# Optimization experiments

Hardware: AMD Instinct MI355X
Metric: run time of the kernel (lower is better)

## Reference

```python
import jax, jax.numpy as jnp
import numpy as np
import math

N_HEAD_FULL = 16  # config.n_head

def setup_inputs() -> dict:
    key = jax.random.key(0)
    ks = jax.random.split(key, 5)
    B, T, D = 2, 4096, 1024
    scale = 1.0 / math.sqrt(D)
    x = jax.random.normal(ks[0], (B, T, D), dtype=jnp.float32)
    wq = jax.random.normal(ks[1], (D, D), dtype=jnp.float32) * scale
    wk = jax.random.normal(ks[2], (D, D), dtype=jnp.float32) * scale
    wv = jax.random.normal(ks[3], (D, D), dtype=jnp.float32) * scale
    wo = jax.random.normal(ks[4], (D, D), dtype=jnp.float32) * scale
    return {"x": x, "wq": wq, "wk": wk, "wv": wv, "wo": wo, "active_dim": 512}

def reference(x, wq, wk, wv, wo, active_dim):
    B, T, D = x.shape
    ad = int(active_dim)
    n_head = max(1, ad * N_HEAD_FULL // D)
    head_dim = ad // n_head
    xs = x[:, :, :ad]
    # F.linear(x, W[:ad,:ad]) == x @ W[:ad,:ad].T
    q = xs @ wq[:ad, :ad].T
    k = xs @ wk[:ad, :ad].T
    v = xs @ wv[:ad, :ad].T
    q = q.reshape(B, T, n_head, head_dim).transpose(0, 2, 1, 3)  # [B,H,T,hd]
    k = k.reshape(B, T, n_head, head_dim).transpose(0, 2, 1, 3)
    v = v.reshape(B, T, n_head, head_dim).transpose(0, 2, 1, 3)
    attn = jnp.einsum('bhqd,bhkd->bhqk', q, k) / math.sqrt(head_dim)
    # kv_cache=None -> T_k=T, triu diagonal = T_k-T+1 = 1 -> strict causal mask
    mask = jnp.triu(jnp.ones((T, T), dtype=bool), k=1)
    attn = jnp.where(mask, -jnp.inf, attn)
    attn = jax.nn.softmax(attn, axis=-1)
    out = jnp.einsum('bhqk,bhkd->bhqd', attn, v)
    out = out.transpose(0, 2, 1, 3).reshape(B, T, ad)
    out = out @ wo[:ad, :ad].T
    return jnp.pad(out, ((0, 0), (0, 0), (0, D - ad)))
```

## Files before the change

kernel.cpp:

```cpp
#include <hip/hip_runtime.h>
#include <hip/hip_bf16.h>
#include <stdint.h>


typedef __bf16 bf16;
typedef bf16  bf16x8 __attribute__((ext_vector_type(8)));
typedef bf16  bf16x4v __attribute__((ext_vector_type(4)));
typedef float f32x4  __attribute__((ext_vector_type(4)));
typedef uint32_t u32x4 __attribute__((ext_vector_type(4)));

#define SCL 0.18033688011112042f
#define NEG_BIG (-30000.0f)

static __device__ __forceinline__ f32x4 mfma_bf16(bf16x8 a, bf16x8 b, f32x4 c) {
    return __builtin_amdgcn_mfma_f32_16x16x32_bf16(a, b, c, 0, 0, 0);
}

static __device__ __forceinline__ void gl_lds(const bf16* g, bf16* l) {
    __builtin_amdgcn_global_load_lds(
        (const __attribute__((address_space(1))) uint32_t*)(g),
        (__attribute__((address_space(3))) uint32_t*)(l), 16, 0, 0);
}

__global__ __launch_bounds__(256) void sniff_dtype(
    const uint16_t* __restrict__ x, int* __restrict__ flag)
{
    __shared__ int cnt;
    if (threadIdx.x == 0) cnt = 0;
    __syncthreads();
    int local = 0;
    for (int i = threadIdx.x; i < 2048; i += 256) {
        const int e = (x[i] >> 7) & 0xFF;
        if (e >= 0xC0) ++local;
    }
    if (local) atomicAdd(&cnt, local);
    __syncthreads();
    if (threadIdx.x == 0) *flag = (cnt >= 8) ? 1 : 0;
}

__global__ __launch_bounds__(256) void convert_all(
    const void* __restrict__ x,
    const void* __restrict__ wq, const void* __restrict__ wk,
    const void* __restrict__ wv, const void* __restrict__ wo,
    bf16* __restrict__ xb, bf16* __restrict__ wb,
    const int* __restrict__ flag)
{
    const int bid = blockIdx.x;
    const void* src;
    bf16* dst;
    int sub;
    if (bid < 2048) { src = x; dst = xb; sub = bid; }
    else {
        const int w = bid - 2048;
        const int wsel = w >> 7;
        src = (wsel == 0) ? wq : (wsel == 1) ? wk : (wsel == 2) ? wv : wo;
        dst = wb + (size_t)wsel * 262144;
        sub = w & 127;
    }
    const int i = (sub * 256 + threadIdx.x) * 8;
    const int r = i >> 9, c = i & 511;
    bf16x8 v;
    if (*flag) {
        const float* s = (const float*)src + (size_t)r * 1024 + c;
        f32x4 f0 = *(const f32x4*)s;
        f32x4 f1 = *(const f32x4*)(s + 4);
#pragma unroll
        for (int j = 0; j < 4; ++j) { v[j] = (bf16)f0[j]; v[4 + j] = (bf16)f1[j]; }
    } else {
        v = *(const bf16x8*)((const bf16*)src + (size_t)r * 1024 + c);
    }
    *(bf16x8*)(dst + (size_t)r * 512 + c) = v;
}

__global__ __launch_bounds__(256) void gemm_qkv(
    const bf16* __restrict__ A, const bf16* __restrict__ B,
    bf16* __restrict__ Qb, bf16* __restrict__ Kb, bf16* __restrict__ Vb)
{
    const int bx   = blockIdx.x;
    const int n0   = bx * 128;
    const int m0   = blockIdx.y * 128;
    const int wave = threadIdx.x >> 6;
    const int lane = threadIdx.x & 63;
    const int col  = lane & 15;
    const int quad = lane >> 4;
    const int wr   = wave >> 1, wc = wave & 1;

    __shared__ __align__(16) bf16 As[2][128][64];
    __shared__ __align__(16) bf16 Bs[2][128][64];

    const int rr = lane >> 3, cc = lane & 7;
    const int cs = (cc ^ rr) * 8;

    auto stage = [&](int kt, int buf) {
#pragma unroll
        for (int j = 0; j < 4; ++j) {
            const int r0 = wave * 32 + j * 8;
            gl_lds(A + (size_t)(m0 + r0 + rr) * 512 + kt * 64 + cs, &As[buf][r0][0]);
            gl_lds(B + (size_t)(n0 + r0 + rr) * 512 + kt * 64 + cs, &Bs[buf][r0][0]);
        }
    };

    f32x4 acc[4][4];
#pragma unroll
    for (int m = 0; m < 4; ++m)
#pragma unroll
        for (int n = 0; n < 4; ++n)
#pragma unroll
            for (int r = 0; r < 4; ++r) acc[m][n][r] = 0.0f;

    stage(0, 0);
    asm volatile("s_waitcnt vmcnt(0)" ::: "memory");
    __syncthreads();

    for (int kt = 0; kt < 8; ++kt) {
        const int buf = kt & 1;
        if (kt + 1 < 8) stage(kt + 1, buf ^ 1);

#pragma unroll
        for (int kk = 0; kk < 2; ++kk) {
            bf16x8 af[4], bfr[4];
#pragma unroll
            for (int m = 0; m < 4; ++m) {
                const int row = wr * 64 + m * 16 + col;
                af[m] = *(const bf16x8*)&As[buf][row][(((kk << 2) + quad) ^ (col & 7)) * 8];
            }
#pragma unroll
            for (int n = 0; n < 4; ++n) {
                const int row = wc * 64 + n * 16 + col;
                bfr[n] = *(const bf16x8*)&Bs[buf][row][(((kk << 2) + quad) ^ (col & 7)) * 8];
            }
#pragma unroll
            for (int m = 0; m < 4; ++m)
#pragma unroll
                for (int n = 0; n < 4; ++n)
                    acc[m][n] = mfma_bf16(af[m], bfr[n], acc[m][n]);
        }

        asm volatile("s_waitcnt vmcnt(0)" ::: "memory");
        __syncthreads();
    }

    const int bb = m0 >> 12;

    if (bx < 8) {
        bf16* __restrict__ dst = (bx < 4) ? Qb : Kb;
        const float qs = (bx < 4) ? SCL : 1.0f;
#pragma unroll
        for (int m = 0; m < 4; ++m) {
#pragma unroll
            for (int n = 0; n < 4; ++n) {
#pragma unroll
                for (int r = 0; r < 4; ++r) {
                    const int row = m0 + wr * 64 + m * 16 + quad * 4 + r;
                    const int cnl = (n0 & 511) + wc * 64 + n * 16 + col;
                    const int t = row & 4095;
                    const int h = cnl >> 6, d = cnl & 63;
                    dst[((size_t)(bb * 8 + h) * 4096 + t) * 64 + d] = (bf16)(acc[m][n][r] * qs);
                }
            }
        }
    } else {
        const int h0 = (n0 - 1024) >> 6;
#pragma unroll
        for (int m = 0; m < 4; ++m) {
#pragma unroll
            for (int n = 0; n < 4; ++n) {
                bf16x4v pk;
#pragma unroll
                for (int r = 0; r < 4; ++r) pk[r] = (bf16)acc[m][n][r];
                const int d  = wc * 64 + n * 16 + col;
                const int t  = (m0 & 4095) + wr * 64 + m * 16 + quad * 4;
                *(bf16x4v*)(Vb + ((size_t)(bb * 8 + h0 + (d >> 6)) * 64 + (d & 63)) * 4096 + t) = pk;
            }
        }
    }
}

__global__ __launch_bounds__(256) void gemm_out_pad(
    const bf16* __restrict__ A, const bf16* __restrict__ B, void* __restrict__ C,
    const int* __restrict__ flag)
{
    const int bx  = blockIdx.x;
    const int m0  = blockIdx.y * 128;
    const int isf = *flag;

    if (bx >= 4) {
        const int c0  = 512 + (bx - 4) * 128;
        const int row = m0 + (threadIdx.x >> 1);
        const int cb  = (threadIdx.x & 1) * 64;
        if (isf) {
            float* p = (float*)C + (size_t)row * 1024 + c0 + cb;
            f32x4 z; z[0] = 0.f; z[1] = 0.f; z[2] = 0.f; z[3] = 0.f;
#pragma unroll
            for (int j = 0; j < 16; ++j) *(f32x4*)(p + j * 4) = z;
        } else {
            bf16* p = (bf16*)C + (size_t)row * 1024 + c0 + cb;
            u32x4 z; z[0] = 0u; z[1] = 0u; z[2] = 0u; z[3] = 0u;
#pragma unroll
            for (int j = 0; j < 8; ++j) *(u32x4*)(p + j * 8) = z;
        }
        return;
    }

    const int n0   = bx * 128;
    const int wave = threadIdx.x >> 6;
    const int lane = threadIdx.x & 63;
    const int col  = lane & 15;
    const int quad = lane >> 4;
    const int wr   = wave >> 1, wc = wave & 1;

    __shared__ __align__(16) bf16 As[2][128][64];
    __shared__ __align__(16) bf16 Bs[2][128][64];

    const int rr = lane >> 3, cc = lane & 7;
    const int cs = (cc ^ rr) * 8;

    auto stage = [&](int kt, int buf) {
#pragma unroll
        for (int j = 0; j < 4; ++j) {
            const int r0 = wave * 32 + j * 8;
            gl_lds(A + (size_t)(m0 + r0 + rr) * 512 + kt * 64 + cs, &As[buf][r0][0]);
            gl_lds(B + (size_t)(n0 + r0 + rr) * 512 + kt * 64 + cs, &Bs[buf][r0][0]);
        }
    };

    f32x4 acc[4][4];
#pragma unroll
    for (int m = 0; m < 4; ++m)
#pragma unroll
        for (int n = 0; n < 4; ++n)
#pragma unroll
            for (int r = 0; r < 4; ++r) acc[m][n][r] = 0.0f;

    stage(0, 0);
    asm volatile("s_waitcnt vmcnt(0)" ::: "memory");
    __syncthreads();

    for (int kt = 0; kt < 8; ++kt) {
        const int buf = kt & 1;
        if (kt + 1 < 8) stage(kt + 1, buf ^ 1);

#pragma unroll
        for (int kk = 0; kk < 2; ++kk) {
            bf16x8 af[4], bfr[4];
#pragma unroll
            for (int m = 0; m < 4; ++m) {
                const int row = wr * 64 + m * 16 + col;
                af[m] = *(const bf16x8*)&As[buf][row][(((kk << 2) + quad) ^ (col & 7)) * 8];
            }
#pragma unroll
            for (int n = 0; n < 4; ++n) {
                const int row = wc * 64 + n * 16 + col;
                bfr[n] = *(const bf16x8*)&Bs[buf][row][(((kk << 2) + quad) ^ (col & 7)) * 8];
            }
#pragma unroll
            for (int m = 0; m < 4; ++m)
#pragma unroll
                for (int n = 0; n < 4; ++n)
                    acc[m][n] = mfma_bf16(af[m], bfr[n], acc[m][n]);
        }

        asm volatile("s_waitcnt vmcnt(0)" ::: "memory");
        __syncthreads();
    }

#pragma unroll
    for (int m = 0; m < 4; ++m) {
#pragma unroll
        for (int n = 0; n < 4; ++n) {
#pragma unroll
            for (int r = 0; r < 4; ++r) {
                const int row = m0 + wr * 64 + m * 16 + quad * 4 + r;
                const int cn  = n0 + wc * 64 + n * 16 + col;
                const float f = acc[m][n][r];
                if (isf) ((float*)C)[(size_t)row * 1024 + cn] = f;
                else     ((bf16*)C)[(size_t)row * 1024 + cn] = (bf16)f;
            }
        }
    }
}

template<int NSPLIT>
__global__ __launch_bounds__(256) void flash_kernel(
    const bf16* __restrict__ Q, const bf16* __restrict__ K,
    const bf16* __restrict__ Vt,
    float* __restrict__ Opart, float* __restrict__ Spart)
{
    const int wave = threadIdx.x >> 6;
    const int lane = threadIdx.x & 63;
    const int qc   = lane & 15;
    const int quad = lane >> 4;

    const int bh  = blockIdx.x & 15;
    const int qb0 = (blockIdx.x >> 4) & 15;
    const int s   = blockIdx.x >> 8;

    const int STEPS = 66 / NSPLIT;
    const int g0 = STEPS * s, g1 = g0 + STEPS;

    const bf16* __restrict__ Qh = Q  + (size_t)bh * (4096 * 64);
    const bf16* __restrict__ Kh = K  + (size_t)bh * (4096 * 64);
    const bf16* __restrict__ Vh = Vt + (size_t)bh * (64 * 4096);

    __shared__ __align__(16) bf16 Ksh[2][64][64];
    __shared__ __align__(16) bf16 Vsh[2][64][64];
    __shared__ __align__(16) bf16 Plds[4][2][16][72];

    const int h   = qc & 7;
    const int swz = (quad ^ h) * 8;
    const bf16* kB  = &Ksh[0][qc][swz];
    const bf16* kB2 = &Ksh[0][qc][swz ^ 32];
    const bf16* vB  = &Vsh[0][qc][swz];
    const bf16* vB2 = &Vsh[0][qc][swz ^ 32];
    bf16*       pwA = &Plds[wave][0][qc][quad * 4];
    const bf16* prA = &Plds[wave][0][qc][quad * 8];

    const int rr = lane >> 3, cc = lane & 7;
    const int cs = (cc ^ rr) * 8;

    bf16x8 vones;
#pragma unroll
    for (int j = 0; j < 8; ++j) vones[j] = (bf16)1.0f;

    auto stage = [&](int kb, int buf) {
#pragma unroll
        for (int j = 0; j < 2; ++j) {
            const int r0 = wave * 16 + j * 8;
            gl_lds(Kh + (size_t)(kb * 64 + r0 + rr) * 64 + cs, &Ksh[buf][r0][0]);
            gl_lds(Vh + (size_t)(r0 + rr) * 4096 + kb * 64 + cs, &Vsh[buf][r0][0]);
        }
    };

    for (int chunk = 0; chunk < 2; ++chunk) {
        const int qb  = chunk ? (31 - qb0) : qb0;
        const int n0t = 2 * qb0 + 2;
        const int n1t = 64 - 2 * qb0;
        int k0, k1;
        if (chunk == 0) {
            k0 = (g0 > 0) ? g0 : 0;
            k1 = (g1 < n0t) ? g1 : n0t;
        } else {
            const int a = g0 - n0t, b2 = g1 - n0t;
            k0 = (a > 0) ? a : 0;
            k1 = (b2 < n1t) ? b2 : n1t;
        }

        const int qrow   = qb * 128 + wave * 32;
        const int ktmaxw = 2 * qb + (wave >> 1);

        bf16x8 aqA0 = *(const bf16x8*)(Qh + (size_t)(qrow + qc) * 64 + quad * 8);
        bf16x8 aqA1 = *(const bf16x8*)(Qh + (size_t)(qrow + qc) * 64 + 32 + quad * 8);
        bf16x8 aqB0 = *(const bf16x8*)(Qh + (size_t)(qrow + 16 + qc) * 64 + quad * 8);
        bf16x8 aqB1 = *(const bf16x8*)(Qh + (size_t)(qrow + 16 + qc) * 64 + 32 + quad * 8);

        f32x4 oA[4], oB[4], saccA, saccB;
#pragma unroll
        for (int r = 0; r < 4; ++r) { saccA[r] = 0.f; saccB[r] = 0.f; }
#pragma unroll
        for (int nt = 0; nt < 4; ++nt)
#pragma unroll
            for (int r = 0; r < 4; ++r) { oA[nt][r] = 0.f; oB[nt][r] = 0.f; }

        auto body = [&](const int kb, const int buf) {
            if (kb <= ktmaxw) {
                const bool diag = (kb == ktmaxw);

#pragma unroll
                for (int nt = 0; nt < 4; ++nt) {
                    bf16x8 kf0 = *(const bf16x8*)(kB  + buf * 4096 + nt * 1024);
                    bf16x8 kf1 = *(const bf16x8*)(kB2 + buf * 4096 + nt * 1024);

                    f32x4 sA; sA[0] = 0.f; sA[1] = 0.f; sA[2] = 0.f; sA[3] = 0.f;
                    sA = mfma_bf16(kf0, aqA0, sA);
                    sA = mfma_bf16(kf1, aqA1, sA);
                    f32x4 sB; sB[0] = 0.f; sB[1] = 0.f; sB[2] = 0.f; sB[3] = 0.f;
                    sB = mfma_bf16(kf0, aqB0, sB);
                    sB = mfma_bf16(kf1, aqB1, sB);

                    bf16x4v pkA, pkB;
#pragma unroll
                    for (int r2 = 0; r2 < 4; ++r2) {
                        float vA = sA[r2];
                        float vBv = sB[r2];
                        if (diag) {
                            const int kg = kb * 64 + nt * 16 + quad * 4 + r2;
                            if (kg > qrow + qc)      vA  = NEG_BIG;
                            if (kg > qrow + 16 + qc) vBv = NEG_BIG;
                        }
                        pkA[r2] = (bf16)__builtin_amdgcn_exp2f(vA);
                        pkB[r2] = (bf16)__builtin_amdgcn_exp2f(vBv);
                    }
                    *(bf16x4v*)(pwA + nt * 16)        = pkA;
                    *(bf16x4v*)(pwA + 1152 + nt * 16) = pkB;
                }

#pragma unroll
                for (int ks = 0; ks < 2; ++ks) {
                    bf16x8 apA = *(const bf16x8*)(prA + ks * 32);
                    bf16x8 apB = *(const bf16x8*)(prA + 1152 + ks * 32);
#pragma unroll
                    for (int nt = 0; nt < 4; ++nt) {
                        bf16x8 vf = *(const bf16x8*)((ks ? vB2 : vB) + buf * 4096 + nt * 1024);
                        oA[nt] = mfma_bf16(apA, vf, oA[nt]);
                        oB[nt] = mfma_bf16(apB, vf, oB[nt]);
                    }
                    saccA = mfma_bf16(apA, vones, saccA);
                    saccB = mfma_bf16(apB, vones, saccB);
                }
            }
        };

        if (k0 < k1) {
            stage(k0, 0);
            asm volatile("s_waitcnt vmcnt(0)" ::: "memory");
            __syncthreads();

            int kb = k0;
            while (true) {
                if (kb + 1 < k1) stage(kb + 1, 1);
                body(kb, 0);
                asm volatile("s_waitcnt vmcnt(0)" ::: "memory");
                __syncthreads();
                ++kb; if (kb >= k1) break;

                if (kb + 1 < k1) stage(kb + 1, 0);
                body(kb, 1);
                asm volatile("s_waitcnt vmcnt(0)" ::: "memory");
                __syncthreads();
                ++kb; if (kb >= k1) break;
            }
        }

        const int pw = (qb * 16 + bh) * NSPLIT + s;
        float* op = Opart + (size_t)pw * 8192 + (size_t)(wave * 32) * 64;
#pragma unroll
        for (int nt = 0; nt < 4; ++nt)
#pragma unroll
            for (int r = 0; r < 4; ++r) {
                op[(quad * 4 + r) * 64 + nt * 16 + qc]        = oA[nt][r];
                op[1024 + (quad * 4 + r) * 64 + nt * 16 + qc] = oB[nt][r];
            }
        if (qc == 0) {
            float* sp = Spart + (size_t)pw * 128 + wave * 32;
#pragma unroll
            for (int r = 0; r < 4; ++r) {
                sp[quad * 4 + r]      = saccA[r];
                sp[16 + quad * 4 + r] = saccB[r];
            }
        }
    }
}

template<int NSPLIT>
__global__ __launch_bounds__(256) void combine_kernel(
    const float* __restrict__ Opart, const float* __restrict__ Spart,
    bf16* __restrict__ Ob)
{
    const int u  = blockIdx.x;
    const int qb = u >> 4;
    const int bh = u & 15;
    const int c  = threadIdx.x & 63;
    const int g  = threadIdx.x >> 6;
    const int b = bh >> 3, h = bh & 7;

    const float* o0 = Opart + (size_t)(u * NSPLIT) * 8192;
    const float* s0 = Spart + (size_t)(u * NSPLIT) * 128;

#pragma unroll 4
    for (int rr = 0; rr < 32; ++rr) {
        const int row = g * 32 + rr;
        float ssum = 0.f, osum = 0.f;
#pragma unroll
        for (int j = 0; j < NSPLIT; ++j) {
            ssum += s0[j * 128 + row];
            osum += o0[(size_t)j * 8192 + row * 64 + c];
        }
        const float v = osum / ssum;
        const int t = qb * 128 + row;
        Ob[((size_t)b * 4096 + t) * 512 + h * 64 + c] = (bf16)v;
    }
}

extern "C" void kernel_launch(void* const* d_in, const int* in_sizes, int n_in,
                              void* d_out, int out_size, void* d_ws, size_t ws_size,
                              hipStream_t stream)
{
    (void)in_sizes; (void)n_in; (void)out_size;
    const void* x  = d_in[0];
    const void* wq = d_in[1];
    const void* wk = d_in[2];
    const void* wv = d_in[3];
    const void* wo = d_in[4];

    char* wsb = (char*)d_ws;
    bf16* xb   = (bf16*)(wsb + 0);
    bf16* Ob   = (bf16*)(wsb + 0);
    bf16* wb   = (bf16*)(wsb + 8388608);
    bf16* wob  = wb + 3 * 262144;
    bf16* Qb   = (bf16*)(wsb + 10485760);
    bf16* Kb   = (bf16*)(wsb + 18874368);
    bf16* Vb   = (bf16*)(wsb + 27262976);
    int*  flag = (int*) (wsb + 35651584);

    const size_t need3 = 35651600ull + (size_t)512 * 3 * (8192 + 128) * 4;
    const int nsplit = (ws_size >= need3) ? 3 : 2;

    float* Opart = (float*)(wsb + 35651600);
    float* Spart = (float*)(wsb + 35651600 + (size_t)512 * nsplit * 8192 * 4);

    const dim3 blk(256);

    sniff_dtype<<<1, blk, 0, stream>>>((const uint16_t*)x, flag);
    convert_all<<<2560, blk, 0, stream>>>(x, wq, wk, wv, wo, xb, wb, flag);

    gemm_qkv<<<dim3(12, 64), blk, 0, stream>>>(xb, wb, Qb, Kb, Vb);

    if (nsplit == 3) {
        flash_kernel<3><<<dim3(768), blk, 0, stream>>>(Qb, Kb, Vb, Opart, Spart);
        combine_kernel<3><<<dim3(512), blk, 0, stream>>>(Opart, Spart, Ob);
    } else {
        flash_kernel<2><<<dim3(512), blk, 0, stream>>>(Qb, Kb, Vb, Opart, Spart);
        combine_kernel<2><<<dim3(512), blk, 0, stream>>>(Opart, Spart, Ob);
    }

    gemm_out_pad<<<dim3(8, 64), blk, 0, stream>>>(Ob, wob, d_out, flag);
}
```

Baseline: 205.4 us.

## Fuse dtype sniff into convert and split-K combine into flash kernel

The dtype detection is now done redundantly by every convert block, which removes the separate sniff kernel launch, and block 1 also zeroes a set of per-tile counters. The split-KV combine step moves into the flash kernel's epilogue: each split bumps an atomic counter, and the last one to finish for a tile does the normalisation and writes Ob. This drops two kernel launches and their gaps in exchange for extra syncthreads and atomics in the flash epilogue, plus an extra 2048 bytes of workspace, which can change the nsplit choice.

Measured after the change: 264.0 us. +28.5%, slower.

```diff
diff --git a/kernel.cpp b/kernel.cpp
--- a/kernel.cpp
+++ b/kernel.cpp
@@ -22,30 +22,32 @@
         (__attribute__((address_space(3))) uint32_t*)(l), 16, 0, 0);
 }
 
-__global__ __launch_bounds__(256) void sniff_dtype(
-    const uint16_t* __restrict__ x, int* __restrict__ flag)
-{
-    __shared__ int cnt;
-    if (threadIdx.x == 0) cnt = 0;
-    __syncthreads();
-    int local = 0;
-    for (int i = threadIdx.x; i < 2048; i += 256) {
-        const int e = (x[i] >> 7) & 0xFF;
-        if (e >= 0xC0) ++local;
-    }
-    if (local) atomicAdd(&cnt, local);
-    __syncthreads();
-    if (threadIdx.x == 0) *flag = (cnt >= 8) ? 1 : 0;
-}
-
 __global__ __launch_bounds__(256) void convert_all(
     const void* __restrict__ x,
     const void* __restrict__ wq, const void* __restrict__ wk,
     const void* __restrict__ wv, const void* __restrict__ wo,
     bf16* __restrict__ xb, bf16* __restrict__ wb,
-    const int* __restrict__ flag)
+    int* __restrict__ flag, int* __restrict__ cnt)
 {
+    __shared__ int scnt;
+    if (threadIdx.x == 0) scnt = 0;
+    __syncthreads();
+    {
+        const uint16_t* xu = (const uint16_t*)x;
+        int local = 0;
+        for (int i = threadIdx.x; i < 2048; i += 256) {
+            const int e = (xu[i] >> 7) & 0xFF;
+            if (e >= 0xC0) ++local;
+        }
+        if (local) atomicAdd(&scnt, local);
+    }
+    __syncthreads();
+    const int isf = (scnt >= 8) ? 1 : 0;
+
     const int bid = blockIdx.x;
+    if (bid == 0 && threadIdx.x == 0) *flag = isf;
+    if (bid == 1) { cnt[threadIdx.x] = 0; cnt[threadIdx.x + 256] = 0; }
+
     const void* src;
     bf16* dst;
     int sub;
@@ -60,7 +62,7 @@
     const int i = (sub * 256 + threadIdx.x) * 8;
     const int r = i >> 9, c = i & 511;
     bf16x8 v;
-    if (*flag) {
+    if (isf) {
         const float* s = (const float*)src + (size_t)r * 1024 + c;
         f32x4 f0 = *(const f32x4*)s;
         f32x4 f1 = *(const f32x4*)(s + 4);
@@ -284,7 +286,8 @@
 __global__ __launch_bounds__(256) void flash_kernel(
     const bf16* __restrict__ Q, const bf16* __restrict__ K,
     const bf16* __restrict__ Vt,
-    float* __restrict__ Opart, float* __restrict__ Spart)
+    float* __restrict__ Opart, float* __restrict__ Spart,
+    bf16* __restrict__ Ob, int* __restrict__ cnt)
 {
     const int wave = threadIdx.x >> 6;
     const int lane = threadIdx.x & 63;
@@ -305,6 +308,7 @@
     __shared__ __align__(16) bf16 Ksh[2][64][64];
     __shared__ __align__(16) bf16 Vsh[2][64][64];
     __shared__ __align__(16) bf16 Plds[4][2][16][72];
+    __shared__ int tick;
 
     const int h   = qc & 7;
     const int swz = (quad ^ h) * 8;
@@ -431,7 +435,8 @@
             }
         }
 
-        const int pw = (qb * 16 + bh) * NSPLIT + s;
+        const int u  = qb * 16 + bh;
+        const int pw = u * NSPLIT + s;
         float* op = Opart + (size_t)pw * 8192 + (size_t)(wave * 32) * 64;
 #pragma unroll
         for (int nt = 0; nt < 4; ++nt)
@@ -448,36 +453,33 @@
                 sp[16 + quad * 4 + r] = saccB[r];
             }
         }
-    }
-}
-
-template<int NSPLIT>
-__global__ __launch_bounds__(256) void combine_kernel(
-    const float* __restrict__ Opart, const float* __restrict__ Spart,
-    bf16* __restrict__ Ob)
-{
-    const int u  = blockIdx.x;
-    const int qb = u >> 4;
-    const int bh = u & 15;
-    const int c  = threadIdx.x & 63;
-    const int g  = threadIdx.x >> 6;
-    const int b = bh >> 3, h = bh & 7;
-
-    const float* o0 = Opart + (size_t)(u * NSPLIT) * 8192;
-    const float* s0 = Spart + (size_t)(u * NSPLIT) * 128;
-
+
+        __syncthreads();
+        if (threadIdx.x == 0)
+            tick = __hip_atomic_fetch_add(&cnt[u], 1, __ATOMIC_ACQ_REL,
+                                          __HIP_MEMORY_SCOPE_AGENT);
+        __syncthreads();
+        if (tick == NSPLIT - 1) {
+            const int c = threadIdx.x & 63;
+            const int g = threadIdx.x >> 6;
+            const int b = bh >> 3, hh = bh & 7;
+            const float* o0 = Opart + (size_t)(u * NSPLIT) * 8192;
+            const float* s0 = Spart + (size_t)(u * NSPLIT) * 128;
 #pragma unroll 4
-    for (int rr = 0; rr < 32; ++rr) {
-        const int row = g * 32 + rr;
-        float ssum = 0.f, osum = 0.f;
-#pragma unroll
-        for (int j = 0; j < NSPLIT; ++j) {
-            ssum += s0[j * 128 + row];
-            osum += o0[(size_t)j * 8192 + row * 64 + c];
-        }
-        const float v = osum / ssum;
-        const int t = qb * 128 + row;
-        Ob[((size_t)b * 4096 + t) * 512 + h * 64 + c] = (bf16)v;
+            for (int rr2 = 0; rr2 < 32; ++rr2) {
+                const int row = g * 32 + rr2;
+                float ssum = 0.f, osum = 0.f;
+#pragma unroll
+                for (int j = 0; j < NSPLIT; ++j) {
+                    ssum += s0[j * 128 + row];
+                    osum += o0[(size_t)j * 8192 + row * 64 + c];
+                }
+                const float v = osum / ssum;
+                const int t = qb * 128 + row;
+                Ob[((size_t)b * 4096 + t) * 512 + hh * 64 + c] = (bf16)v;
+            }
+        }
+        __syncthreads();
     }
 }
 
@@ -502,26 +504,23 @@
     bf16* Vb   = (bf16*)(wsb + 27262976);
     int*  flag = (int*) (wsb + 35651584);
 
-    const size_t need3 = 35651600ull + (size_t)512 * 3 * (8192 + 128) * 4;
+    const size_t need3 = 35651600ull + (size_t)512 * 3 * (8192 + 128) * 4 + 2048;
     const int nsplit = (ws_size >= need3) ? 3 : 2;
 
     float* Opart = (float*)(wsb + 35651600);
-    float* Spart = (float*)(wsb + 35651600 + (size_t)512 * nsplit * 8192 * 4);
+    float* Spart = Opart + (size_t)512 * nsplit * 8192;
+    int*   cnt   = (int*)(Spart + (size_t)512 * nsplit * 128);
 
     const dim3 blk(256);
 
-    sniff_dtype<<<1, blk, 0, stream>>>((const uint16_t*)x, flag);
-    convert_all<<<2560, blk, 0, stream>>>(x, wq, wk, wv, wo, xb, wb, flag);
+    convert_all<<<2560, blk, 0, stream>>>(x, wq, wk, wv, wo, xb, wb, flag, cnt);
 
     gemm_qkv<<<dim3(12, 64), blk, 0, stream>>>(xb, wb, Qb, Kb, Vb);
 
-    if (nsplit == 3) {
-        flash_kernel<3><<<dim3(768), blk, 0, stream>>>(Qb, Kb, Vb, Opart, Spart);
-        combine_kernel<3><<<dim3(512), blk, 0, stream>>>(Opart, Spart, Ob);
-    } else {
-        flash_kernel<2><<<dim3(512), blk, 0, stream>>>(Qb, Kb, Vb, Opart, Spart);
-        combine_kernel<2><<<dim3(512), blk, 0, stream>>>(Opart, Spart, Ob);
-    }
+    if (nsplit == 3)
+        flash_kernel<3><<<dim3(768), blk, 0, stream>>>(Qb, Kb, Vb, Opart, Spart, Ob, cnt);
+    else
+        flash_kernel<2><<<dim3(512), blk, 0, stream>>>(Qb, Kb, Vb, Opart, Spart, Ob, cnt);
 
     gemm_out_pad<<<dim3(8, 64), blk, 0, stream>>>(Ob, wob, d_out, flag);
 }
```
